# Optimization experiments

Hardware: AMD Instinct MI355X
Metric: run time of the kernel (lower is better)

The kernel has to match this reference:

```python
import jax, jax.numpy as jnp
import numpy as np

HEAD_NUM = 16
EMB_DIM = 1024
PROJ_DIM = 1024
CONTEXT_LEN = 2048
HEAD_DIM = PROJ_DIM // HEAD_NUM


def setup_inputs() -> dict:
    key = jax.random.key(0)
    k_x, k_q, k_k, k_v, k_o = jax.random.split(key, 5)
    scale = 0.02
    X_emb = jax.random.normal(k_x, (2, CONTEXT_LEN, EMB_DIM), dtype=jnp.float32)
    W_q = jax.random.normal(k_q, (EMB_DIM, PROJ_DIM), dtype=jnp.float32) * scale
    W_k = jax.random.normal(k_k, (EMB_DIM, PROJ_DIM), dtype=jnp.float32) * scale
    W_v = jax.random.normal(k_v, (EMB_DIM, PROJ_DIM), dtype=jnp.float32) * scale
    W_out = jax.random.normal(k_o, (PROJ_DIM, PROJ_DIM), dtype=jnp.float32) * scale
    return {"X_emb": X_emb, "W_q": W_q, "W_k": W_k, "W_v": W_v, "W_out": W_out}


def reference(X_emb, W_q, W_k, W_v, W_out):
    B, S, _ = X_emb.shape
    H, D = HEAD_NUM, HEAD_DIM
    # QKV projections (no bias), split into heads: [B, H, S, D]
    q = (X_emb @ W_q).reshape(B, S, H, D).transpose(0, 2, 1, 3)
    k = (X_emb @ W_k).reshape(B, S, H, D).transpose(0, 2, 1, 3)
    v = (X_emb @ W_v).reshape(B, S, H, D).transpose(0, 2, 1, 3)
    # Raw scores [B, H, S, S]; causal mask applied BEFORE scaling (as in source;
    # -inf is invariant under the subsequent division so math matches).
    scores = jnp.einsum("bhqd,bhkd->bhqk", q, k)
    causal = jnp.triu(jnp.ones((S, S), dtype=bool), k=1)  # True above diagonal
    scores = jnp.where(causal, -jnp.inf, scores)
    scores = scores / jnp.asarray(np.sqrt(D), dtype=scores.dtype)
    att_w = jax.nn.softmax(scores, axis=-1)
    # dropout_rate = 0.0 -> identity
    ctx = jnp.einsum("bhqk,bhkd->bhqd", att_w, v)
    ctx = ctx.transpose(0, 2, 1, 3).reshape(B, S, H * D)
    return ctx @ W_out
```

## Files before the change

### kernel.cpp

```cpp
#include <hip/hip_runtime.h>
#include <stdint.h>

#define SEQ   2048
#define EMB   1024
#define PROJ  1024
#define HEADS 16
#define HD    64
#define BATCH 2
#define MROWS (BATCH * SEQ)
#define QKVN  3072

typedef __attribute__((ext_vector_type(8))) __bf16 bf16x8;
typedef __attribute__((ext_vector_type(4))) __bf16 bf16x4;
typedef __attribute__((ext_vector_type(4))) float  f32x4;

static __device__ __forceinline__ __bf16 f2b(float f) {
  union { float f; uint32_t u; } a; a.f = f;
  uint32_t r = a.u + 0x7FFFu + ((a.u >> 16) & 1u);
  union { uint16_t u; __bf16 b; } o; o.u = (uint16_t)(r >> 16);
  return o.b;
}

#define GLOAD_LDS16(gsrc, ldst)                                                \
  __builtin_amdgcn_global_load_lds(                                            \
      (const __attribute__((address_space(1))) void*)(gsrc),                   \
      (__attribute__((address_space(3))) void*)(ldst), 16, 0, 0)

__global__ void cast_f32_bf16(const float* __restrict__ in,
                              __bf16* __restrict__ out, int n) {
  int i = (blockIdx.x * blockDim.x + threadIdx.x) * 4;
  if (i + 3 < n) {
    float4 v = *reinterpret_cast<const float4*>(in + i);
    bf16x4 o;
    o[0] = f2b(v.x); o[1] = f2b(v.y); o[2] = f2b(v.z); o[3] = f2b(v.w);
    *reinterpret_cast<bf16x4*>(out + i) = o;
  }
}

__global__ void transpose_cast(const float* __restrict__ W0, const float* __restrict__ W1,
                               const float* __restrict__ W2, const float* __restrict__ W3,
                               __bf16* __restrict__ Tqkv, __bf16* __restrict__ To) {
  const float* W; __bf16* T;
  switch (blockIdx.z) {
    case 0: W = W0; T = Tqkv;                       break;
    case 1: W = W1; T = Tqkv + (size_t)1024 * 1024; break;
    case 2: W = W2; T = Tqkv + (size_t)2048 * 1024; break;
    default: W = W3; T = To;                        break;
  }
  __shared__ float tile[32][33];
  int k0 = blockIdx.x * 32, n0 = blockIdx.y * 32;
  int tx = threadIdx.x & 31, ty = threadIdx.x >> 5;
#pragma unroll
  for (int r = ty; r < 32; r += 8)
    tile[r][tx] = W[(size_t)(k0 + r) * 1024 + n0 + tx];
  __syncthreads();
#pragma unroll
  for (int r = ty; r < 32; r += 8)
    T[(size_t)(n0 + r) * 1024 + k0 + tx] = f2b(tile[tx][r]);
}

template <int BM, bool OUT_BF16, bool SCALE_Q>
__global__ __launch_bounds__(256) void gemm_bt(const __bf16* __restrict__ A,
                                               const __bf16* __restrict__ Bt,
                                               void* __restrict__ Cout,
                                               int M, int N, int K) {
  constexpr int MI = BM / 32;
  __shared__ __align__(16) __bf16 As[BM * 32];
  __shared__ __align__(16) __bf16 Bs[128 * 32];
  const int t = threadIdx.x;
  const int lane = t & 63, w = t >> 6;
  const int g = lane >> 4, l15 = lane & 15;
  const int m0 = blockIdx.x * BM, n0 = blockIdx.y * 128;
  const int wr = w >> 1, wc = w & 1;

  f32x4 acc[MI][4];
#pragma unroll
  for (int i = 0; i < MI; i++)
#pragma unroll
    for (int j = 0; j < 4; j++) acc[i][j] = {0.f, 0.f, 0.f, 0.f};

  for (int k0 = 0; k0 < K; k0 += 32) {
    __syncthreads();
#pragma unroll
    for (int c = t; c < BM * 4; c += 256)
      GLOAD_LDS16(A + (size_t)(m0 + (c >> 2)) * K + k0 + (c & 3) * 8, As + c * 8);
#pragma unroll
    for (int c = t; c < 512; c += 256)
      GLOAD_LDS16(Bt + (size_t)(n0 + (c >> 2)) * K + k0 + (c & 3) * 8, Bs + c * 8);
    __syncthreads();

    bf16x8 af[MI], bfr[4];
#pragma unroll
    for (int mi = 0; mi < MI; mi++)
      af[mi] = *reinterpret_cast<const bf16x8*>(As + (wr * (BM / 2) + mi * 16 + l15) * 32 + g * 8);
#pragma unroll
    for (int ni = 0; ni < 4; ni++)
      bfr[ni] = *reinterpret_cast<const bf16x8*>(Bs + (wc * 64 + ni * 16 + l15) * 32 + g * 8);
#pragma unroll
    for (int mi = 0; mi < MI; mi++)
#pragma unroll
      for (int ni = 0; ni < 4; ni++)
        acc[mi][ni] = __builtin_amdgcn_mfma_f32_16x16x32_bf16(af[mi], bfr[ni], acc[mi][ni], 0, 0, 0);
  }

#pragma unroll
  for (int mi = 0; mi < MI; mi++)
#pragma unroll
    for (int ni = 0; ni < 4; ni++) {
      int row = m0 + wr * (BM / 2) + mi * 16 + g * 4;
      int col = n0 + wc * 64 + ni * 16 + l15;
#pragma unroll
      for (int r = 0; r < 4; r++) {
        float v = acc[mi][ni][r];
        if (SCALE_Q && col < 1024) v *= 0.125f;
        if (OUT_BF16)
          ((__bf16*)Cout)[(size_t)(row + r) * N + col] = f2b(v);
        else
          ((float*)Cout)[(size_t)(row + r) * N + col] = v;
      }
    }
}

__global__ void v_transpose(const __bf16* __restrict__ QKV, __bf16* __restrict__ Vt) {
  const int sb = blockIdx.x, bh = blockIdx.y;
  const int lane = threadIdx.x & 63, w = threadIdx.x >> 6;
  const int b = bh >> 4, h = bh & 15;
  const int s = sb * 64 + lane;
  const __bf16* src = QKV + (size_t)b * SEQ * QKVN + (size_t)s * QKVN + 2048 + h * 64 + w * 16;
  bf16x8 v0 = *reinterpret_cast<const bf16x8*>(src);
  bf16x8 v1 = *reinterpret_cast<const bf16x8*>(src + 8);
  __bf16* dst = Vt + ((size_t)bh * 64 + w * 16) * 2048 + s;
#pragma unroll
  for (int j = 0; j < 8; j++) dst[(size_t)j * 2048] = v0[j];
#pragma unroll
  for (int j = 0; j < 8; j++) dst[(size_t)(8 + j) * 2048] = v1[j];
}

__global__ __launch_bounds__(256, 2) void attn_fwd(const __bf16* __restrict__ QKV,
                                                   const __bf16* __restrict__ Vt,
                                                   __bf16* __restrict__ ctx) {
  const int id = blockIdx.x;
  const int bh = (id & 7) * 4 + ((id >> 3) & 3);
  const int pair = id >> 5;
  const int b = bh >> 4, h = bh & 15;
  const int tid = threadIdx.x, lane = tid & 63, w = tid >> 6;
  const int g = lane >> 4, l15 = lane & 15;

  __shared__ __align__(16) __bf16 Ks[2][64 * 64];
  __shared__ __align__(16) __bf16 Vs[2][64 * 64];
  __shared__ __align__(16) __bf16 P_lds[4][16][72];

  const __bf16* Qg  = QKV + (size_t)b * SEQ * QKVN + h * 64;
  const __bf16* Kg  = Qg + 1024;
  const __bf16* VtH = Vt + (size_t)bh * 64 * 2048;
  __bf16* Cg = ctx + (size_t)b * SEQ * 1024 + h * 64;

  const int r0 = tid >> 3, j0 = tid & 7;
  const int r1 = r0 + 32;
  const int ls0 = r0 * 64 + ((j0 ^ (r0 & 7)) * 8);
  const int ls1 = r1 * 64 + ((j0 ^ (r1 & 7)) * 8);
  const size_t gk0 = (size_t)r0 * QKVN + j0 * 8;
  const size_t gk1 = (size_t)r1 * QKVN + j0 * 8;
  const size_t gv0 = (size_t)r0 * 2048 + j0 * 8;
  const size_t gv1 = (size_t)r1 * 2048 + j0 * 8;
  const int xw = l15 & 7;

  for (int mem = 0; mem < 2; ++mem) {
    const int mi = mem ? (31 - pair) : pair;
    const int qw = mi * 64 + 16 * w;
    const int Tm = mi + 1;

    bf16x8 qf[2];
#pragma unroll
    for (int ks = 0; ks < 2; ks++)
      qf[ks] = *reinterpret_cast<const bf16x8*>(
          Qg + (size_t)(qw + l15) * QKVN + ks * 32 + g * 8);

    f32x4 acco[4];
    float mrun = -1e30f, lrun = 0.f;
#pragma unroll
    for (int nd = 0; nd < 4; nd++) acco[nd] = {0.f, 0.f, 0.f, 0.f};

    {
      bf16x8 ka = *reinterpret_cast<const bf16x8*>(Kg + gk0);
      bf16x8 kb = *reinterpret_cast<const bf16x8*>(Kg + gk1);
      bf16x8 va = *reinterpret_cast<const bf16x8*>(VtH + gv0);
      bf16x8 vc = *reinterpret_cast<const bf16x8*>(VtH + gv1);
      *reinterpret_cast<bf16x8*>(Ks[0] + ls0) = ka;
      *reinterpret_cast<bf16x8*>(Ks[0] + ls1) = kb;
      *reinterpret_cast<bf16x8*>(Vs[0] + ls0) = va;
      *reinterpret_cast<bf16x8*>(Vs[0] + ls1) = vc;
    }
    __syncthreads();

    for (int it = 0; it < Tm; ++it) {
      const int cur = it & 1, nxt = cur ^ 1;
      const bool hn = (it + 1 < Tm);
      bf16x8 ka, kb, va, vc;
      if (hn) {
        const size_t kvn = (size_t)(it + 1) * 64;
        ka = *reinterpret_cast<const bf16x8*>(Kg + kvn * QKVN + gk0);
        kb = *reinterpret_cast<const bf16x8*>(Kg + kvn * QKVN + gk1);
        va = *reinterpret_cast<const bf16x8*>(VtH + kvn + gv0);
        vc = *reinterpret_cast<const bf16x8*>(VtH + kvn + gv1);
      }

      {
        const int kv0 = it * 64;
        const bool diag = (it == Tm - 1);
        const __bf16* Kc = Ks[cur];
        const __bf16* Vc = Vs[cur];

        bf16x8 kf[4][2], vb[4][2];
#pragma unroll
        for (int nb = 0; nb < 4; nb++) {
          const int row = (nb * 16 + l15) * 64;
#pragma unroll
          for (int ks = 0; ks < 2; ks++) {
            const int co = ((ks * 4 + g) ^ xw) * 8;
            kf[nb][ks] = *reinterpret_cast<const bf16x8*>(Kc + row + co);
            vb[nb][ks] = *reinterpret_cast<const bf16x8*>(Vc + row + co);
          }
        }

        f32x4 accS[4];
#pragma unroll
        for (int nb = 0; nb < 4; nb++) accS[nb] = {0.f, 0.f, 0.f, 0.f};
#pragma unroll
        for (int nb = 0; nb < 4; nb++) {
          accS[nb] = __builtin_amdgcn_mfma_f32_16x16x32_bf16(kf[nb][0], qf[0], accS[nb], 0, 0, 0);
          accS[nb] = __builtin_amdgcn_mfma_f32_16x16x32_bf16(kf[nb][1], qf[1], accS[nb], 0, 0, 0);
        }

        if (diag) {
          const int qi = qw + l15;
#pragma unroll
          for (int nb = 0; nb < 4; nb++)
#pragma unroll
            for (int r = 0; r < 4; r++) {
              int kvi = kv0 + nb * 16 + g * 4 + r;
              if (kvi > qi) accS[nb][r] = -1e30f;
            }
        }

        {
          float pmax = -1e30f;
#pragma unroll
          for (int nb = 0; nb < 4; nb++)
#pragma unroll
            for (int r = 0; r < 4; r++) pmax = fmaxf(pmax, accS[nb][r]);
          pmax = fmaxf(pmax, __shfl_xor(pmax, 16));
          pmax = fmaxf(pmax, __shfl_xor(pmax, 32));
          if (!__all(pmax <= mrun + 8.0f)) {
            float mnew = fmaxf(mrun, pmax);
            float corr = __expf(mrun - mnew);
            mrun = mnew;
            lrun *= corr;
#pragma unroll
            for (int r = 0; r < 4; r++) {
              float cr = __shfl(corr, (g << 4) + (g << 2) + r);
#pragma unroll
              for (int nd = 0; nd < 4; nd++) acco[nd][r] *= cr;
            }
          }
          float lsum = 0.f;
#pragma unroll
          for (int nb = 0; nb < 4; nb++) {
            bf16x4 pk;
#pragma unroll
            for (int r = 0; r < 4; r++) {
              float pv = __expf(accS[nb][r] - mrun);
              lsum += pv;
              pk[r] = (__bf16)pv;
            }
            *reinterpret_cast<bf16x4*>(&P_lds[w][l15][nb * 16 + g * 4]) = pk;
          }
          lsum += __shfl_xor(lsum, 16);
          lsum += __shfl_xor(lsum, 32);
          lrun += lsum;
        }

        {
          bf16x8 pa0 = *reinterpret_cast<const bf16x8*>(&P_lds[w][l15][g * 8]);
          bf16x8 pa1 = *reinterpret_cast<const bf16x8*>(&P_lds[w][l15][32 + g * 8]);
#pragma unroll
          for (int nd = 0; nd < 4; nd++) {
            acco[nd] = __builtin_amdgcn_mfma_f32_16x16x32_bf16(pa0, vb[nd][0], acco[nd], 0, 0, 0);
            acco[nd] = __builtin_amdgcn_mfma_f32_16x16x32_bf16(pa1, vb[nd][1], acco[nd], 0, 0, 0);
          }
        }
      }

      if (hn) {
        *reinterpret_cast<bf16x8*>(Ks[nxt] + ls0) = ka;
        *reinterpret_cast<bf16x8*>(Ks[nxt] + ls1) = kb;
        *reinterpret_cast<bf16x8*>(Vs[nxt] + ls0) = va;
        *reinterpret_cast<bf16x8*>(Vs[nxt] + ls1) = vc;
      }
      __syncthreads();
    }

    {
      float inv = 1.0f / lrun;
#pragma unroll
      for (int r = 0; r < 4; r++) {
        float ir = __shfl(inv, (g << 4) + (g << 2) + r);
        int qrow = qw + g * 4 + r;
#pragma unroll
        for (int nd = 0; nd < 4; nd++)
          Cg[(size_t)qrow * 1024 + nd * 16 + l15] = (__bf16)(acco[nd][r] * ir);
      }
    }
  }
}

extern "C" void kernel_launch(void* const* d_in, const int* in_sizes, int n_in,
                              void* d_out, int out_size, void* d_ws, size_t ws_size,
                              hipStream_t stream) {
  const float* X  = (const float*)d_in[0];
  const float* Wq = (const float*)d_in[1];
  const float* Wk = (const float*)d_in[2];
  const float* Wv = (const float*)d_in[3];
  const float* Wo = (const float*)d_in[4];
  float* out = (float*)d_out;

  uint8_t* ws = (uint8_t*)d_ws;
  size_t off = 0;
  const size_t actBytes = (size_t)MROWS * 1024 * 2;
  __bf16* Xb    = (__bf16*)(ws + off); off += actBytes;
  __bf16* WqkvT = (__bf16*)(ws + off); off += (size_t)QKVN * 1024 * 2;
  __bf16* WoT   = (__bf16*)(ws + off); off += (size_t)1024 * 1024 * 2;
  __bf16* QKV   = (__bf16*)(ws + off); off += (size_t)MROWS * QKVN * 2;
  __bf16* Vt    = (__bf16*)(ws + off); off += actBytes;
  __bf16* Cb    = Xb;

  cast_f32_bf16<<<dim3(MROWS * 1024 / 4 / 256), dim3(256), 0, stream>>>(X, Xb, MROWS * 1024);
  transpose_cast<<<dim3(32, 32, 4), dim3(256), 0, stream>>>(Wq, Wk, Wv, Wo, WqkvT, WoT);

  gemm_bt<128, true, true><<<dim3(MROWS / 128, QKVN / 128), dim3(256), 0, stream>>>(
      Xb, WqkvT, QKV, MROWS, QKVN, EMB);

  v_transpose<<<dim3(SEQ / 64, BATCH * HEADS), dim3(256), 0, stream>>>(QKV, Vt);
  attn_fwd<<<dim3(512), dim3(256), 0, stream>>>(QKV, Vt, Cb);

  gemm_bt<64, false, false><<<dim3(MROWS / 64, PROJ / 128), dim3(256), 0, stream>>>(
      Cb, WoT, out, MROWS, PROJ, PROJ);
}
```

Measured before the change: 115.9 us.

## Fuse V transpose into QKV GEMM epilogue and use 128-wide KV tiles in attention

The QKV GEMM epilogue now writes the V columns straight into the transposed Vt layout, so the separate v_transpose kernel launch and its extra pass over V are gone. The attention kernel now stages 128-key K/V tiles per iteration and processes each one as two 64-key halves. This halves the number of barriers and global-to-LDS rounds per query block, at the cost of doubled LDS footprint (about 64KB of K/V buffers) and more registers for prefetch, which may reduce occupancy at 2 blocks/SM.

```diff
diff --git a/kernel.cpp b/kernel.cpp
--- a/kernel.cpp
+++ b/kernel.cpp
@@ -59,10 +59,11 @@
     T[(size_t)(n0 + r) * 1024 + k0 + tx] = f2b(tile[tx][r]);
 }
 
-template <int BM, bool OUT_BF16, bool SCALE_Q>
+template <int BM, bool OUT_BF16, bool SCALE_Q, bool VSPLIT>
 __global__ __launch_bounds__(256) void gemm_bt(const __bf16* __restrict__ A,
                                                const __bf16* __restrict__ Bt,
                                                void* __restrict__ Cout,
+                                               __bf16* __restrict__ vt,
                                                int M, int N, int K) {
   constexpr int MI = BM / 32;
   __shared__ __align__(16) __bf16 As[BM * 32];
@@ -109,31 +110,25 @@
     for (int ni = 0; ni < 4; ni++) {
       int row = m0 + wr * (BM / 2) + mi * 16 + g * 4;
       int col = n0 + wc * 64 + ni * 16 + l15;
-#pragma unroll
-      for (int r = 0; r < 4; r++) {
-        float v = acc[mi][ni][r];
-        if (SCALE_Q && col < 1024) v *= 0.125f;
-        if (OUT_BF16)
-          ((__bf16*)Cout)[(size_t)(row + r) * N + col] = f2b(v);
-        else
-          ((float*)Cout)[(size_t)(row + r) * N + col] = v;
+      if (VSPLIT && col >= 2048) {
+        int hd = col - 2048;
+        int bb = row >> 11, ss = row & 2047;
+        bf16x4 v4;
+#pragma unroll
+        for (int r = 0; r < 4; r++) v4[r] = f2b(acc[mi][ni][r]);
+        *reinterpret_cast<bf16x4*>(vt + ((size_t)((bb * 16 + (hd >> 6)) * 64 + (hd & 63))) * 2048 + ss) = v4;
+      } else {
+#pragma unroll
+        for (int r = 0; r < 4; r++) {
+          float v = acc[mi][ni][r];
+          if (SCALE_Q && col < 1024) v *= 0.125f;
+          if (OUT_BF16)
+            ((__bf16*)Cout)[(size_t)(row + r) * N + col] = f2b(v);
+          else
+            ((float*)Cout)[(size_t)(row + r) * N + col] = v;
+        }
       }
     }
-}
-
-__global__ void v_transpose(const __bf16* __restrict__ QKV, __bf16* __restrict__ Vt) {
-  const int sb = blockIdx.x, bh = blockIdx.y;
-  const int lane = threadIdx.x & 63, w = threadIdx.x >> 6;
-  const int b = bh >> 4, h = bh & 15;
-  const int s = sb * 64 + lane;
-  const __bf16* src = QKV + (size_t)b * SEQ * QKVN + (size_t)s * QKVN + 2048 + h * 64 + w * 16;
-  bf16x8 v0 = *reinterpret_cast<const bf16x8*>(src);
-  bf16x8 v1 = *reinterpret_cast<const bf16x8*>(src + 8);
-  __bf16* dst = Vt + ((size_t)bh * 64 + w * 16) * 2048 + s;
-#pragma unroll
-  for (int j = 0; j < 8; j++) dst[(size_t)j * 2048] = v0[j];
-#pragma unroll
-  for (int j = 0; j < 8; j++) dst[(size_t)(8 + j) * 2048] = v1[j];
 }
 
 __global__ __launch_bounds__(256, 2) void attn_fwd(const __bf16* __restrict__ QKV,
@@ -146,8 +141,8 @@
   const int tid = threadIdx.x, lane = tid & 63, w = tid >> 6;
   const int g = lane >> 4, l15 = lane & 15;
 
-  __shared__ __align__(16) __bf16 Ks[2][64 * 64];
-  __shared__ __align__(16) __bf16 Vs[2][64 * 64];
+  __shared__ __align__(16) __bf16 Ks[2][128 * 64];
+  __shared__ __align__(16) __bf16 Vs[2][64 * 128];
   __shared__ __align__(16) __bf16 P_lds[4][16][72];
 
   const __bf16* Qg  = QKV + (size_t)b * SEQ * QKVN + h * 64;
@@ -155,20 +150,13 @@
   const __bf16* VtH = Vt + (size_t)bh * 64 * 2048;
   __bf16* Cg = ctx + (size_t)b * SEQ * 1024 + h * 64;
 
-  const int r0 = tid >> 3, j0 = tid & 7;
-  const int r1 = r0 + 32;
-  const int ls0 = r0 * 64 + ((j0 ^ (r0 & 7)) * 8);
-  const int ls1 = r1 * 64 + ((j0 ^ (r1 & 7)) * 8);
-  const size_t gk0 = (size_t)r0 * QKVN + j0 * 8;
-  const size_t gk1 = (size_t)r1 * QKVN + j0 * 8;
-  const size_t gv0 = (size_t)r0 * 2048 + j0 * 8;
-  const size_t gv1 = (size_t)r1 * 2048 + j0 * 8;
   const int xw = l15 & 7;
 
   for (int mem = 0; mem < 2; ++mem) {
     const int mi = mem ? (31 - pair) : pair;
     const int qw = mi * 64 + 16 * w;
-    const int Tm = mi + 1;
+    const int qi = qw + l15;
+    const int Tt = (mi + 2) >> 1;
 
     bf16x8 qf[2];
 #pragma unroll
@@ -182,120 +170,127 @@
     for (int nd = 0; nd < 4; nd++) acco[nd] = {0.f, 0.f, 0.f, 0.f};
 
     {
-      bf16x8 ka = *reinterpret_cast<const bf16x8*>(Kg + gk0);
-      bf16x8 kb = *reinterpret_cast<const bf16x8*>(Kg + gk1);
-      bf16x8 va = *reinterpret_cast<const bf16x8*>(VtH + gv0);
-      bf16x8 vc = *reinterpret_cast<const bf16x8*>(VtH + gv1);
-      *reinterpret_cast<bf16x8*>(Ks[0] + ls0) = ka;
-      *reinterpret_cast<bf16x8*>(Ks[0] + ls1) = kb;
-      *reinterpret_cast<bf16x8*>(Vs[0] + ls0) = va;
-      *reinterpret_cast<bf16x8*>(Vs[0] + ls1) = vc;
+#pragma unroll
+      for (int k = 0; k < 4; k++) {
+        const int c = tid + 256 * k;
+        const int rk = c >> 3, jk = c & 7;
+        const int rv = c >> 4, jv = c & 15;
+        bf16x8 kv = *reinterpret_cast<const bf16x8*>(Kg + (size_t)rk * QKVN + jk * 8);
+        bf16x8 vv = *reinterpret_cast<const bf16x8*>(VtH + (size_t)rv * 2048 + jv * 8);
+        *reinterpret_cast<bf16x8*>(Ks[0] + rk * 64 + ((jk ^ (rk & 7)) * 8)) = kv;
+        *reinterpret_cast<bf16x8*>(Vs[0] + rv * 128 + ((jv ^ (rv & 7)) * 8)) = vv;
+      }
     }
     __syncthreads();
 
-    for (int it = 0; it < Tm; ++it) {
+    for (int it = 0; it < Tt; ++it) {
       const int cur = it & 1, nxt = cur ^ 1;
-      const bool hn = (it + 1 < Tm);
-      bf16x8 ka, kb, va, vc;
+      const bool hn = (it + 1 < Tt);
+      bf16x8 skv[4], svv[4];
       if (hn) {
-        const size_t kvn = (size_t)(it + 1) * 64;
-        ka = *reinterpret_cast<const bf16x8*>(Kg + kvn * QKVN + gk0);
-        kb = *reinterpret_cast<const bf16x8*>(Kg + kvn * QKVN + gk1);
-        va = *reinterpret_cast<const bf16x8*>(VtH + kvn + gv0);
-        vc = *reinterpret_cast<const bf16x8*>(VtH + kvn + gv1);
-      }
-
-      {
-        const int kv0 = it * 64;
-        const bool diag = (it == Tm - 1);
-        const __bf16* Kc = Ks[cur];
-        const __bf16* Vc = Vs[cur];
-
-        bf16x8 kf[4][2], vb[4][2];
-#pragma unroll
-        for (int nb = 0; nb < 4; nb++) {
-          const int row = (nb * 16 + l15) * 64;
-#pragma unroll
-          for (int ks = 0; ks < 2; ks++) {
-            const int co = ((ks * 4 + g) ^ xw) * 8;
-            kf[nb][ks] = *reinterpret_cast<const bf16x8*>(Kc + row + co);
-            vb[nb][ks] = *reinterpret_cast<const bf16x8*>(Vc + row + co);
+        const size_t kvn = (size_t)(it + 1) * 128;
+#pragma unroll
+        for (int k = 0; k < 4; k++) {
+          const int c = tid + 256 * k;
+          const int rk = c >> 3, jk = c & 7;
+          const int rv = c >> 4, jv = c & 15;
+          skv[k] = *reinterpret_cast<const bf16x8*>(Kg + (kvn + rk) * QKVN + jk * 8);
+          svv[k] = *reinterpret_cast<const bf16x8*>(VtH + (size_t)rv * 2048 + kvn + jv * 8);
+        }
+      }
+
+      const __bf16* Kc = Ks[cur];
+      const __bf16* Vc = Vs[cur];
+#pragma unroll
+      for (int hf = 0; hf < 2; hf++) {
+        const int vv = it * 2 + hf;
+        if (vv <= mi) {
+          const int kv0 = vv * 64;
+          const bool maskme = (vv == mi);
+
+          f32x4 accS[4];
+#pragma unroll
+          for (int nb = 0; nb < 4; nb++) accS[nb] = {0.f, 0.f, 0.f, 0.f};
+#pragma unroll
+          for (int nb = 0; nb < 4; nb++) {
+            const int row = (hf * 64 + nb * 16 + l15) * 64;
+            bf16x8 kf0 = *reinterpret_cast<const bf16x8*>(Kc + row + ((g ^ xw) * 8));
+            bf16x8 kf1 = *reinterpret_cast<const bf16x8*>(Kc + row + (((4 + g) ^ xw) * 8));
+            accS[nb] = __builtin_amdgcn_mfma_f32_16x16x32_bf16(kf0, qf[0], accS[nb], 0, 0, 0);
+            accS[nb] = __builtin_amdgcn_mfma_f32_16x16x32_bf16(kf1, qf[1], accS[nb], 0, 0, 0);
+          }
+
+          if (maskme) {
+#pragma unroll
+            for (int nb = 0; nb < 4; nb++)
+#pragma unroll
+              for (int r = 0; r < 4; r++) {
+                int kvi = kv0 + nb * 16 + g * 4 + r;
+                if (kvi > qi) accS[nb][r] = -1e30f;
+              }
+          }
+
+          {
+            float pmax = -1e30f;
+#pragma unroll
+            for (int nb = 0; nb < 4; nb++)
+#pragma unroll
+              for (int r = 0; r < 4; r++) pmax = fmaxf(pmax, accS[nb][r]);
+            pmax = fmaxf(pmax, __shfl_xor(pmax, 16));
+            pmax = fmaxf(pmax, __shfl_xor(pmax, 32));
+            if (!__all(pmax <= mrun + 8.0f)) {
+              float mnew = fmaxf(mrun, pmax);
+              float corr = __expf(mrun - mnew);
+              mrun = mnew;
+              lrun *= corr;
+#pragma unroll
+              for (int r = 0; r < 4; r++) {
+                float cr = __shfl(corr, (g << 4) + (g << 2) + r);
+#pragma unroll
+                for (int nd = 0; nd < 4; nd++) acco[nd][r] *= cr;
+              }
+            }
+            float lsum = 0.f;
+#pragma unroll
+            for (int nb = 0; nb < 4; nb++) {
+              bf16x4 pk;
+#pragma unroll
+              for (int r = 0; r < 4; r++) {
+                float pv = __expf(accS[nb][r] - mrun);
+                lsum += pv;
+                pk[r] = (__bf16)pv;
+              }
+              *reinterpret_cast<bf16x4*>(&P_lds[w][l15][nb * 16 + g * 4]) = pk;
+            }
+            lsum += __shfl_xor(lsum, 16);
+            lsum += __shfl_xor(lsum, 32);
+            lrun += lsum;
+          }
+
+          {
+            bf16x8 pa0 = *reinterpret_cast<const bf16x8*>(&P_lds[w][l15][g * 8]);
+            bf16x8 pa1 = *reinterpret_cast<const bf16x8*>(&P_lds[w][l15][32 + g * 8]);
+#pragma unroll
+            for (int nd = 0; nd < 4; nd++) {
+              const int row = (nd * 16 + l15) * 128;
+              bf16x8 vb0 = *reinterpret_cast<const bf16x8*>(Vc + row + (((hf * 8 + g) ^ xw) * 8));
+              bf16x8 vb1 = *reinterpret_cast<const bf16x8*>(Vc + row + (((hf * 8 + 4 + g) ^ xw) * 8));
+              acco[nd] = __builtin_amdgcn_mfma_f32_16x16x32_bf16(pa0, vb0, acco[nd], 0, 0, 0);
+              acco[nd] = __builtin_amdgcn_mfma_f32_16x16x32_bf16(pa1, vb1, acco[nd], 0, 0, 0);
+            }
           }
         }
-
-        f32x4 accS[4];
-#pragma unroll
-        for (int nb = 0; nb < 4; nb++) accS[nb] = {0.f, 0.f, 0.f, 0.f};
-#pragma unroll
-        for (int nb = 0; nb < 4; nb++) {
-          accS[nb] = __builtin_amdgcn_mfma_f32_16x16x32_bf16(kf[nb][0], qf[0], accS[nb], 0, 0, 0);
-          accS[nb] = __builtin_amdgcn_mfma_f32_16x16x32_bf16(kf[nb][1], qf[1], accS[nb], 0, 0, 0);
+      }
+
+      if (hn) {
+#pragma unroll
+        for (int k = 0; k < 4; k++) {
+          const int c = tid + 256 * k;
+          const int rk = c >> 3, jk = c & 7;
+          const int rv = c >> 4, jv = c & 15;
+          *reinterpret_cast<bf16x8*>(Ks[nxt] + rk * 64 + ((jk ^ (rk & 7)) * 8)) = skv[k];
+          *reinterpret_cast<bf16x8*>(Vs[nxt] + rv * 128 + ((jv ^ (rv & 7)) * 8)) = svv[k];
         }
-
-        if (diag) {
-          const int qi = qw + l15;
-#pragma unroll
-          for (int nb = 0; nb < 4; nb++)
-#pragma unroll
-            for (int r = 0; r < 4; r++) {
-              int kvi = kv0 + nb * 16 + g * 4 + r;
-              if (kvi > qi) accS[nb][r] = -1e30f;
-            }
-        }
-
-        {
-          float pmax = -1e30f;
-#pragma unroll
-          for (int nb = 0; nb < 4; nb++)
-#pragma unroll
-            for (int r = 0; r < 4; r++) pmax = fmaxf(pmax, accS[nb][r]);
-          pmax = fmaxf(pmax, __shfl_xor(pmax, 16));
-          pmax = fmaxf(pmax, __shfl_xor(pmax, 32));
-          if (!__all(pmax <= mrun + 8.0f)) {
-            float mnew = fmaxf(mrun, pmax);
-            float corr = __expf(mrun - mnew);
-            mrun = mnew;
-            lrun *= corr;
-#pragma unroll
-            for (int r = 0; r < 4; r++) {
-              float cr = __shfl(corr, (g << 4) + (g << 2) + r);
-#pragma unroll
-              for (int nd = 0; nd < 4; nd++) acco[nd][r] *= cr;
-            }
-          }
-          float lsum = 0.f;
-#pragma unroll
-          for (int nb = 0; nb < 4; nb++) {
-            bf16x4 pk;
-#pragma unroll
-            for (int r = 0; r < 4; r++) {
-              float pv = __expf(accS[nb][r] - mrun);
-              lsum += pv;
-              pk[r] = (__bf16)pv;
-            }
-            *reinterpret_cast<bf16x4*>(&P_lds[w][l15][nb * 16 + g * 4]) = pk;
-          }
-          lsum += __shfl_xor(lsum, 16);
-          lsum += __shfl_xor(lsum, 32);
-          lrun += lsum;
-        }
-
-        {
-          bf16x8 pa0 = *reinterpret_cast<const bf16x8*>(&P_lds[w][l15][g * 8]);
-          bf16x8 pa1 = *reinterpret_cast<const bf16x8*>(&P_lds[w][l15][32 + g * 8]);
-#pragma unroll
-          for (int nd = 0; nd < 4; nd++) {
-            acco[nd] = __builtin_amdgcn_mfma_f32_16x16x32_bf16(pa0, vb[nd][0], acco[nd], 0, 0, 0);
-            acco[nd] = __builtin_amdgcn_mfma_f32_16x16x32_bf16(pa1, vb[nd][1], acco[nd], 0, 0, 0);
-          }
-        }
-      }
-
-      if (hn) {
-        *reinterpret_cast<bf16x8*>(Ks[nxt] + ls0) = ka;
-        *reinterpret_cast<bf16x8*>(Ks[nxt] + ls1) = kb;
-        *reinterpret_cast<bf16x8*>(Vs[nxt] + ls0) = va;
-        *reinterpret_cast<bf16x8*>(Vs[nxt] + ls1) = vc;
       }
       __syncthreads();
     }
@@ -337,12 +332,11 @@
   cast_f32_bf16<<<dim3(MROWS * 1024 / 4 / 256), dim3(256), 0, stream>>>(X, Xb, MROWS * 1024);
   transpose_cast<<<dim3(32, 32, 4), dim3(256), 0, stream>>>(Wq, Wk, Wv, Wo, WqkvT, WoT);
 
-  gemm_bt<128, true, true><<<dim3(MROWS / 128, QKVN / 128), dim3(256), 0, stream>>>(
-      Xb, WqkvT, QKV, MROWS, QKVN, EMB);
-
-  v_transpose<<<dim3(SEQ / 64, BATCH * HEADS), dim3(256), 0, stream>>>(QKV, Vt);
+  gemm_bt<128, true, true, true><<<dim3(MROWS / 128, QKVN / 128), dim3(256), 0, stream>>>(
+      Xb, WqkvT, QKV, Vt, MROWS, QKVN, EMB);
+
   attn_fwd<<<dim3(512), dim3(256), 0, stream>>>(QKV, Vt, Cb);
 
-  gemm_bt<64, false, false><<<dim3(MROWS / 64, PROJ / 128), dim3(256), 0, stream>>>(
-      Cb, WoT, out, MROWS, PROJ, PROJ);
-}
+  gemm_bt<64, false, false, false><<<dim3(MROWS / 64, PROJ / 128), dim3(256), 0, stream>>>(
+      Cb, WoT, out, nullptr, MROWS, PROJ, PROJ);
+}
```

After: 112.5 us. 1.03x faster.

## Fuse V transpose into QKV GEMM epilogue and unpair attention blocks

Applied to the files above, without the earlier changes.

The QKV GEMM epilogue writes V columns directly into a per-head transposed Vt buffer, eliminating the separate v_transpose kernel launch and its extra read/write pass. The attention kernel switches from processing a balanced pair of query tiles per block to one tile per block with 1024 blocks ordered longest-first, relying on the hardware scheduler for load balance. The output projection GEMM uses a 128-row tile, which halves its grid and may reduce occupancy.

```diff
diff --git a/kernel.cpp b/kernel.cpp
--- a/kernel.cpp
+++ b/kernel.cpp
@@ -59,10 +59,11 @@
     T[(size_t)(n0 + r) * 1024 + k0 + tx] = f2b(tile[tx][r]);
 }
 
-template <int BM, bool OUT_BF16, bool SCALE_Q>
+template <int BM, bool OUT_BF16, bool SCALE_Q, bool VSPLIT>
 __global__ __launch_bounds__(256) void gemm_bt(const __bf16* __restrict__ A,
                                                const __bf16* __restrict__ Bt,
                                                void* __restrict__ Cout,
+                                               __bf16* __restrict__ vt,
                                                int M, int N, int K) {
   constexpr int MI = BM / 32;
   __shared__ __align__(16) __bf16 As[BM * 32];
@@ -109,31 +110,25 @@
     for (int ni = 0; ni < 4; ni++) {
       int row = m0 + wr * (BM / 2) + mi * 16 + g * 4;
       int col = n0 + wc * 64 + ni * 16 + l15;
-#pragma unroll
-      for (int r = 0; r < 4; r++) {
-        float v = acc[mi][ni][r];
-        if (SCALE_Q && col < 1024) v *= 0.125f;
-        if (OUT_BF16)
-          ((__bf16*)Cout)[(size_t)(row + r) * N + col] = f2b(v);
-        else
-          ((float*)Cout)[(size_t)(row + r) * N + col] = v;
-      }
-    }
-}
-
-__global__ void v_transpose(const __bf16* __restrict__ QKV, __bf16* __restrict__ Vt) {
-  const int sb = blockIdx.x, bh = blockIdx.y;
-  const int lane = threadIdx.x & 63, w = threadIdx.x >> 6;
-  const int b = bh >> 4, h = bh & 15;
-  const int s = sb * 64 + lane;
-  const __bf16* src = QKV + (size_t)b * SEQ * QKVN + (size_t)s * QKVN + 2048 + h * 64 + w * 16;
-  bf16x8 v0 = *reinterpret_cast<const bf16x8*>(src);
-  bf16x8 v1 = *reinterpret_cast<const bf16x8*>(src + 8);
-  __bf16* dst = Vt + ((size_t)bh * 64 + w * 16) * 2048 + s;
-#pragma unroll
-  for (int j = 0; j < 8; j++) dst[(size_t)j * 2048] = v0[j];
-#pragma unroll
-  for (int j = 0; j < 8; j++) dst[(size_t)(8 + j) * 2048] = v1[j];
+      if (VSPLIT && col >= 2048) {
+        int hd = col - 2048;
+        int bb = row >> 11, ss = row & 2047;
+        bf16x4 v4;
+#pragma unroll
+        for (int r = 0; r < 4; r++) v4[r] = f2b(acc[mi][ni][r]);
+        *reinterpret_cast<bf16x4*>(vt + ((size_t)((bb * 16 + (hd >> 6)) * 64 + (hd & 63))) * 2048 + ss) = v4;
+      } else {
+#pragma unroll
+        for (int r = 0; r < 4; r++) {
+          float v = acc[mi][ni][r];
+          if (SCALE_Q && col < 1024) v *= 0.125f;
+          if (OUT_BF16)
+            ((__bf16*)Cout)[(size_t)(row + r) * N + col] = f2b(v);
+          else
+            ((float*)Cout)[(size_t)(row + r) * N + col] = v;
+        }
+      }
+    }
 }
 
 __global__ __launch_bounds__(256, 2) void attn_fwd(const __bf16* __restrict__ QKV,
@@ -141,7 +136,7 @@
                                                    __bf16* __restrict__ ctx) {
   const int id = blockIdx.x;
   const int bh = (id & 7) * 4 + ((id >> 3) & 3);
-  const int pair = id >> 5;
+  const int mi = 31 - (id >> 5);
   const int b = bh >> 4, h = bh & 15;
   const int tid = threadIdx.x, lane = tid & 63, w = tid >> 6;
   const int g = lane >> 4, l15 = lane & 15;
@@ -165,151 +160,148 @@
   const size_t gv1 = (size_t)r1 * 2048 + j0 * 8;
   const int xw = l15 & 7;
 
-  for (int mem = 0; mem < 2; ++mem) {
-    const int mi = mem ? (31 - pair) : pair;
-    const int qw = mi * 64 + 16 * w;
-    const int Tm = mi + 1;
-
-    bf16x8 qf[2];
-#pragma unroll
-    for (int ks = 0; ks < 2; ks++)
-      qf[ks] = *reinterpret_cast<const bf16x8*>(
-          Qg + (size_t)(qw + l15) * QKVN + ks * 32 + g * 8);
-
-    f32x4 acco[4];
-    float mrun = -1e30f, lrun = 0.f;
-#pragma unroll
-    for (int nd = 0; nd < 4; nd++) acco[nd] = {0.f, 0.f, 0.f, 0.f};
+  const int qw = mi * 64 + 16 * w;
+  const int Tm = mi + 1;
+
+  bf16x8 qf[2];
+#pragma unroll
+  for (int ks = 0; ks < 2; ks++)
+    qf[ks] = *reinterpret_cast<const bf16x8*>(
+        Qg + (size_t)(qw + l15) * QKVN + ks * 32 + g * 8);
+
+  f32x4 acco[4];
+  float mrun = -1e30f, lrun = 0.f;
+#pragma unroll
+  for (int nd = 0; nd < 4; nd++) acco[nd] = {0.f, 0.f, 0.f, 0.f};
+
+  {
+    bf16x8 ka = *reinterpret_cast<const bf16x8*>(Kg + gk0);
+    bf16x8 kb = *reinterpret_cast<const bf16x8*>(Kg + gk1);
+    bf16x8 va = *reinterpret_cast<const bf16x8*>(VtH + gv0);
+    bf16x8 vc = *reinterpret_cast<const bf16x8*>(VtH + gv1);
+    *reinterpret_cast<bf16x8*>(Ks[0] + ls0) = ka;
+    *reinterpret_cast<bf16x8*>(Ks[0] + ls1) = kb;
+    *reinterpret_cast<bf16x8*>(Vs[0] + ls0) = va;
+    *reinterpret_cast<bf16x8*>(Vs[0] + ls1) = vc;
+  }
+  __syncthreads();
+
+  for (int it = 0; it < Tm; ++it) {
+    const int cur = it & 1, nxt = cur ^ 1;
+    const bool hn = (it + 1 < Tm);
+    bf16x8 ka, kb, va, vc;
+    if (hn) {
+      const size_t kvn = (size_t)(it + 1) * 64;
+      ka = *reinterpret_cast<const bf16x8*>(Kg + kvn * QKVN + gk0);
+      kb = *reinterpret_cast<const bf16x8*>(Kg + kvn * QKVN + gk1);
+      va = *reinterpret_cast<const bf16x8*>(VtH + kvn + gv0);
+      vc = *reinterpret_cast<const bf16x8*>(VtH + kvn + gv1);
+    }
 
     {
-      bf16x8 ka = *reinterpret_cast<const bf16x8*>(Kg + gk0);
-      bf16x8 kb = *reinterpret_cast<const bf16x8*>(Kg + gk1);
-      bf16x8 va = *reinterpret_cast<const bf16x8*>(VtH + gv0);
-      bf16x8 vc = *reinterpret_cast<const bf16x8*>(VtH + gv1);
-      *reinterpret_cast<bf16x8*>(Ks[0] + ls0) = ka;
-      *reinterpret_cast<bf16x8*>(Ks[0] + ls1) = kb;
-      *reinterpret_cast<bf16x8*>(Vs[0] + ls0) = va;
-      *reinterpret_cast<bf16x8*>(Vs[0] + ls1) = vc;
+      const int kv0 = it * 64;
+      const bool diag = (it == Tm - 1);
+      const __bf16* Kc = Ks[cur];
+      const __bf16* Vc = Vs[cur];
+
+      bf16x8 kf[4][2], vb[4][2];
+#pragma unroll
+      for (int nb = 0; nb < 4; nb++) {
+        const int row = (nb * 16 + l15) * 64;
+#pragma unroll
+        for (int ks = 0; ks < 2; ks++) {
+          const int co = ((ks * 4 + g) ^ xw) * 8;
+          kf[nb][ks] = *reinterpret_cast<const bf16x8*>(Kc + row + co);
+          vb[nb][ks] = *reinterpret_cast<const bf16x8*>(Vc + row + co);
+        }
+      }
+
+      f32x4 accS[4];
+#pragma unroll
+      for (int nb = 0; nb < 4; nb++) accS[nb] = {0.f, 0.f, 0.f, 0.f};
+#pragma unroll
+      for (int nb = 0; nb < 4; nb++) {
+        accS[nb] = __builtin_amdgcn_mfma_f32_16x16x32_bf16(kf[nb][0], qf[0], accS[nb], 0, 0, 0);
+        accS[nb] = __builtin_amdgcn_mfma_f32_16x16x32_bf16(kf[nb][1], qf[1], accS[nb], 0, 0, 0);
+      }
+
+      if (diag) {
+        const int qi = qw + l15;
+#pragma unroll
+        for (int nb = 0; nb < 4; nb++)
+#pragma unroll
+          for (int r = 0; r < 4; r++) {
+            int kvi = kv0 + nb * 16 + g * 4 + r;
+            if (kvi > qi) accS[nb][r] = -1e30f;
+          }
+      }
+
+      {
+        float pmax = -1e30f;
+#pragma unroll
+        for (int nb = 0; nb < 4; nb++)
+#pragma unroll
+          for (int r = 0; r < 4; r++) pmax = fmaxf(pmax, accS[nb][r]);
+        pmax = fmaxf(pmax, __shfl_xor(pmax, 16));
+        pmax = fmaxf(pmax, __shfl_xor(pmax, 32));
+        if (!__all(pmax <= mrun + 8.0f)) {
+          float mnew = fmaxf(mrun, pmax);
+          float corr = __expf(mrun - mnew);
+          mrun = mnew;
+          lrun *= corr;
+#pragma unroll
+          for (int r = 0; r < 4; r++) {
+            float cr = __shfl(corr, (g << 4) + (g << 2) + r);
+#pragma unroll
+            for (int nd = 0; nd < 4; nd++) acco[nd][r] *= cr;
+          }
+        }
+        float lsum = 0.f;
+#pragma unroll
+        for (int nb = 0; nb < 4; nb++) {
+          bf16x4 pk;
+#pragma unroll
+          for (int r = 0; r < 4; r++) {
+            float pv = __expf(accS[nb][r] - mrun);
+            lsum += pv;
+            pk[r] = (__bf16)pv;
+          }
+          *reinterpret_cast<bf16x4*>(&P_lds[w][l15][nb * 16 + g * 4]) = pk;
+        }
+        lsum += __shfl_xor(lsum, 16);
+        lsum += __shfl_xor(lsum, 32);
+        lrun += lsum;
+      }
+
+      {
+        bf16x8 pa0 = *reinterpret_cast<const bf16x8*>(&P_lds[w][l15][g * 8]);
+        bf16x8 pa1 = *reinterpret_cast<const bf16x8*>(&P_lds[w][l15][32 + g * 8]);
+#pragma unroll
+        for (int nd = 0; nd < 4; nd++) {
+          acco[nd] = __builtin_amdgcn_mfma_f32_16x16x32_bf16(pa0, vb[nd][0], acco[nd], 0, 0, 0);
+          acco[nd] = __builtin_amdgcn_mfma_f32_16x16x32_bf16(pa1, vb[nd][1], acco[nd], 0, 0, 0);
+        }
+      }
+    }
+
+    if (hn) {
+      *reinterpret_cast<bf16x8*>(Ks[nxt] + ls0) = ka;
+      *reinterpret_cast<bf16x8*>(Ks[nxt] + ls1) = kb;
+      *reinterpret_cast<bf16x8*>(Vs[nxt] + ls0) = va;
+      *reinterpret_cast<bf16x8*>(Vs[nxt] + ls1) = vc;
     }
     __syncthreads();
-
-    for (int it = 0; it < Tm; ++it) {
-      const int cur = it & 1, nxt = cur ^ 1;
-      const bool hn = (it + 1 < Tm);
-      bf16x8 ka, kb, va, vc;
-      if (hn) {
-        const size_t kvn = (size_t)(it + 1) * 64;
-        ka = *reinterpret_cast<const bf16x8*>(Kg + kvn * QKVN + gk0);
-        kb = *reinterpret_cast<const bf16x8*>(Kg + kvn * QKVN + gk1);
-        va = *reinterpret_cast<const bf16x8*>(VtH + kvn + gv0);
-        vc = *reinterpret_cast<const bf16x8*>(VtH + kvn + gv1);
-      }
-
-      {
-        const int kv0 = it * 64;
-        const bool diag = (it == Tm - 1);
-        const __bf16* Kc = Ks[cur];
-        const __bf16* Vc = Vs[cur];
-
-        bf16x8 kf[4][2], vb[4][2];
-#pragma unroll
-        for (int nb = 0; nb < 4; nb++) {
-          const int row = (nb * 16 + l15) * 64;
-#pragma unroll
-          for (int ks = 0; ks < 2; ks++) {
-            const int co = ((ks * 4 + g) ^ xw) * 8;
-            kf[nb][ks] = *reinterpret_cast<const bf16x8*>(Kc + row + co);
-            vb[nb][ks] = *reinterpret_cast<const bf16x8*>(Vc + row + co);
-          }
-        }
-
-        f32x4 accS[4];
-#pragma unroll
-        for (int nb = 0; nb < 4; nb++) accS[nb] = {0.f, 0.f, 0.f, 0.f};
-#pragma unroll
-        for (int nb = 0; nb < 4; nb++) {
-          accS[nb] = __builtin_amdgcn_mfma_f32_16x16x32_bf16(kf[nb][0], qf[0], accS[nb], 0, 0, 0);
-          accS[nb] = __builtin_amdgcn_mfma_f32_16x16x32_bf16(kf[nb][1], qf[1], accS[nb], 0, 0, 0);
-        }
-
-        if (diag) {
-          const int qi = qw + l15;
-#pragma unroll
-          for (int nb = 0; nb < 4; nb++)
-#pragma unroll
-            for (int r = 0; r < 4; r++) {
-              int kvi = kv0 + nb * 16 + g * 4 + r;
-              if (kvi > qi) accS[nb][r] = -1e30f;
-            }
-        }
-
-        {
-          float pmax = -1e30f;
-#pragma unroll
-          for (int nb = 0; nb < 4; nb++)
-#pragma unroll
-            for (int r = 0; r < 4; r++) pmax = fmaxf(pmax, accS[nb][r]);
-          pmax = fmaxf(pmax, __shfl_xor(pmax, 16));
-          pmax = fmaxf(pmax, __shfl_xor(pmax, 32));
-          if (!__all(pmax <= mrun + 8.0f)) {
-            float mnew = fmaxf(mrun, pmax);
-            float corr = __expf(mrun - mnew);
-            mrun = mnew;
-            lrun *= corr;
-#pragma unroll
-            for (int r = 0; r < 4; r++) {
-              float cr = __shfl(corr, (g << 4) + (g << 2) + r);
-#pragma unroll
-              for (int nd = 0; nd < 4; nd++) acco[nd][r] *= cr;
-            }
-          }
-          float lsum = 0.f;
-#pragma unroll
-          for (int nb = 0; nb < 4; nb++) {
-            bf16x4 pk;
-#pragma unroll
-            for (int r = 0; r < 4; r++) {
-              float pv = __expf(accS[nb][r] - mrun);
-              lsum += pv;
-              pk[r] = (__bf16)pv;
-            }
-            *reinterpret_cast<bf16x4*>(&P_lds[w][l15][nb * 16 + g * 4]) = pk;
-          }
-          lsum += __shfl_xor(lsum, 16);
-          lsum += __shfl_xor(lsum, 32);
-          lrun += lsum;
-        }
-
-        {
-          bf16x8 pa0 = *reinterpret_cast<const bf16x8*>(&P_lds[w][l15][g * 8]);
-          bf16x8 pa1 = *reinterpret_cast<const bf16x8*>(&P_lds[w][l15][32 + g * 8]);
-#pragma unroll
-          for (int nd = 0; nd < 4; nd++) {
-            acco[nd] = __builtin_amdgcn_mfma_f32_16x16x32_bf16(pa0, vb[nd][0], acco[nd], 0, 0, 0);
-            acco[nd] = __builtin_amdgcn_mfma_f32_16x16x32_bf16(pa1, vb[nd][1], acco[nd], 0, 0, 0);
-          }
-        }
-      }
-
-      if (hn) {
-        *reinterpret_cast<bf16x8*>(Ks[nxt] + ls0) = ka;
-        *reinterpret_cast<bf16x8*>(Ks[nxt] + ls1) = kb;
-        *reinterpret_cast<bf16x8*>(Vs[nxt] + ls0) = va;
-        *reinterpret_cast<bf16x8*>(Vs[nxt] + ls1) = vc;
-      }
-      __syncthreads();
-    }
-
-    {
-      float inv = 1.0f / lrun;
-#pragma unroll
-      for (int r = 0; r < 4; r++) {
-        float ir = __shfl(inv, (g << 4) + (g << 2) + r);
-        int qrow = qw + g * 4 + r;
-#pragma unroll
-        for (int nd = 0; nd < 4; nd++)
-          Cg[(size_t)qrow * 1024 + nd * 16 + l15] = (__bf16)(acco[nd][r] * ir);
-      }
+  }
+
+  {
+    float inv = 1.0f / lrun;
+#pragma unroll
+    for (int r = 0; r < 4; r++) {
+      float ir = __shfl(inv, (g << 4) + (g << 2) + r);
+      int qrow = qw + g * 4 + r;
+#pragma unroll
+      for (int nd = 0; nd < 4; nd++)
+        Cg[(size_t)qrow * 1024 + nd * 16 + l15] = (__bf16)(acco[nd][r] * ir);
     }
   }
 }
@@ -337,12 +329,11 @@
   cast_f32_bf16<<<dim3(MROWS * 1024 / 4 / 256), dim3(256), 0, stream>>>(X, Xb, MROWS * 1024);
   transpose_cast<<<dim3(32, 32, 4), dim3(256), 0, stream>>>(Wq, Wk, Wv, Wo, WqkvT, WoT);
 
-  gemm_bt<128, true, true><<<dim3(MROWS / 128, QKVN / 128), dim3(256), 0, stream>>>(
-      Xb, WqkvT, QKV, MROWS, QKVN, EMB);
-
-  v_transpose<<<dim3(SEQ / 64, BATCH * HEADS), dim3(256), 0, stream>>>(QKV, Vt);
-  attn_fwd<<<dim3(512), dim3(256), 0, stream>>>(QKV, Vt, Cb);
-
-  gemm_bt<64, false, false><<<dim3(MROWS / 64, PROJ / 128), dim3(256), 0, stream>>>(
-      Cb, WoT, out, MROWS, PROJ, PROJ);
-}
+  gemm_bt<128, true, true, true><<<dim3(MROWS / 128, QKVN / 128), dim3(256), 0, stream>>>(
+      Xb, WqkvT, QKV, Vt, MROWS, QKVN, EMB);
+
+  attn_fwd<<<dim3(1024), dim3(256), 0, stream>>>(QKV, Vt, Cb);
+
+  gemm_bt<128, false, false, false><<<dim3(MROWS / 128, PROJ / 128), dim3(256), 0, stream>>>(
+      Cb, WoT, out, nullptr, MROWS, PROJ, PROJ);
+}
```

Result: faster. 113.3 us (-2.2%).
